# Performance work log

Hardware: AMD Instinct MI355X
Metric: run time of the kernel (lower is better)

The kernel has to match this reference:

```python
import jax, jax.numpy as jnp
import numpy as np
from jax import lax

SEQ, BATCH, INPUT, HIDDEN = 2048, 32, 256, 256


def setup_inputs() -> dict:
    key = jax.random.key(0)
    k1, k2, k3 = jax.random.split(key, 3)
    scale = 1.0 / np.sqrt(HIDDEN)
    return {
        "input": jax.random.normal(k1, (SEQ, BATCH, INPUT), dtype=jnp.float32),
        "W_ih": jax.random.normal(k2, (3 * HIDDEN, INPUT), dtype=jnp.float32) * scale,
        "W_hh": jax.random.normal(k3, (3 * HIDDEN, HIDDEN), dtype=jnp.float32) * scale,
        "b_ih": jnp.zeros((3 * HIDDEN,), dtype=jnp.float32),
        "b_hh": jnp.zeros((3 * HIDDEN,), dtype=jnp.float32),
    }


def reference(input, W_ih, W_hh, b_ih, b_hh):
    """Single-layer unidirectional CustomGRU forward.

    Faithful to the torch module, including its quirk: the n-gate gets the
    W_hh_n @ h contribution twice (once un-gated via `gates`, once gated by r).
    Returns (output [S,B,H], h_n [1,B,H]).
    """
    H = W_hh.shape[0] // 3
    W_hn = W_hh[2 * H:]  # [H, H]
    # Precompute input projections for all timesteps (same math, batched GEMM).
    x_proj = jnp.einsum('sbi,gi->sbg', input, W_ih) + b_ih + b_hh  # [S,B,3H]

    def step(h, xp):
        gates = xp + h @ W_hh.T  # [B, 3H]
        r, z, n = jnp.split(gates, 3, axis=1)
        r = jax.nn.sigmoid(r)
        z = jax.nn.sigmoid(z)
        n = jnp.tanh(n + r * (h @ W_hn.T))
        h_new = (1.0 - z) * n + z * h
        return h_new, h_new

    h0 = jnp.zeros((input.shape[1], H), dtype=input.dtype)
    h_last, output = lax.scan(step, h0, x_proj)
    return output, h_last[None, :, :]
```

## Files before the change

kernel.cpp:

```cpp
#include <hip/hip_runtime.h>
#include <stdint.h>
#include <stddef.h>

#define S_LEN 2048
#define BATCH 32
#define NIN   256
#define NH    256
#define NG    768

typedef _Float16 half2_t __attribute__((ext_vector_type(2)));
typedef _Float16 half8_t __attribute__((ext_vector_type(8)));
typedef int      int16v  __attribute__((ext_vector_type(16)));

#if __has_builtin(__builtin_amdgcn_exp2f)
#define EXP2F(x) __builtin_amdgcn_exp2f(x)
#else
#define EXP2F(x) exp2f(x)
#endif

static __device__ __forceinline__ float fdot2(half2_t a, half2_t b, float c) {
  return __builtin_amdgcn_fdot2(a, b, c, false);
}
static __device__ __forceinline__ half2_t pack2(float lo, float hi) {
  half2_t r; r[0] = (_Float16)lo; r[1] = (_Float16)hi; return r;
}
static __device__ __forceinline__ float sigmoid_fast(float x) {
  float e = EXP2F(-1.44269504088896340736f * x);
  return 1.0f / (1.0f + e);
}
static __device__ __forceinline__ float tanh_fast(float x) {
  float e = EXP2F(2.88539008177792681472f * x);
  return 1.0f - 2.0f / (1.0f + e);
}

static __device__ __forceinline__ float quad_sum(float v) {
  int y1 = __builtin_amdgcn_mov_dpp(__builtin_bit_cast(int, v), 0xB1, 0xF, 0xF, true);
  float s = v + __builtin_bit_cast(float, y1);
  int y2 = __builtin_amdgcn_mov_dpp(__builtin_bit_cast(int, s), 0x4E, 0xF, 0xF, true);
  return s + __builtin_bit_cast(float, y2);
}

#define BH(x)    __builtin_bit_cast(half2_t, (x))
#define BW(W, e) __builtin_bit_cast(half2_t, (int)((W)[e]))

#define DOT16(W, i0) do {                                                     \
    int4 q0 = hls[(i0) + 0], q1 = hls[(i0) + 1];                              \
    int4 q2 = hls[(i0) + 2], q3 = hls[(i0) + 3];                              \
    a0 = fdot2(BW(W, 0),  BH(q0.x), a0); a1 = fdot2(BW(W, 1),  BH(q0.y), a1);\
    a2 = fdot2(BW(W, 2),  BH(q0.z), a2); a3 = fdot2(BW(W, 3),  BH(q0.w), a3);\
    a0 = fdot2(BW(W, 4),  BH(q1.x), a0); a1 = fdot2(BW(W, 5),  BH(q1.y), a1);\
    a2 = fdot2(BW(W, 6),  BH(q1.z), a2); a3 = fdot2(BW(W, 7),  BH(q1.w), a3);\
    a0 = fdot2(BW(W, 8),  BH(q2.x), a0); a1 = fdot2(BW(W, 9),  BH(q2.y), a1);\
    a2 = fdot2(BW(W, 10), BH(q2.z), a2); a3 = fdot2(BW(W, 11), BH(q2.w), a3);\
    a0 = fdot2(BW(W, 12), BH(q3.x), a0); a1 = fdot2(BW(W, 13), BH(q3.y), a1);\
    a2 = fdot2(BW(W, 14), BH(q3.z), a2); a3 = fdot2(BW(W, 15), BH(q3.w), a3);\
  } while (0)

#define DOT6(q, U0, U1, U2, U3, U4, U5, o) do {                               \
    a0 = fdot2(BW(U0,(o)+0), BH(q.x), a0); a1 = fdot2(BW(U1,(o)+0), BH(q.x), a1);\
    a2 = fdot2(BW(U2,(o)+0), BH(q.x), a2); a3 = fdot2(BW(U3,(o)+0), BH(q.x), a3);\
    a4 = fdot2(BW(U4,(o)+0), BH(q.x), a4); a5 = fdot2(BW(U5,(o)+0), BH(q.x), a5);\
    a0 = fdot2(BW(U0,(o)+1), BH(q.y), a0); a1 = fdot2(BW(U1,(o)+1), BH(q.y), a1);\
    a2 = fdot2(BW(U2,(o)+1), BH(q.y), a2); a3 = fdot2(BW(U3,(o)+1), BH(q.y), a3);\
    a4 = fdot2(BW(U4,(o)+1), BH(q.y), a4); a5 = fdot2(BW(U5,(o)+1), BH(q.y), a5);\
    a0 = fdot2(BW(U0,(o)+2), BH(q.z), a0); a1 = fdot2(BW(U1,(o)+2), BH(q.z), a1);\
    a2 = fdot2(BW(U2,(o)+2), BH(q.z), a2); a3 = fdot2(BW(U3,(o)+2), BH(q.z), a3);\
    a4 = fdot2(BW(U4,(o)+2), BH(q.z), a4); a5 = fdot2(BW(U5,(o)+2), BH(q.z), a5);\
    a0 = fdot2(BW(U0,(o)+3), BH(q.w), a0); a1 = fdot2(BW(U1,(o)+3), BH(q.w), a1);\
    a2 = fdot2(BW(U2,(o)+3), BH(q.w), a2); a3 = fdot2(BW(U3,(o)+3), BH(q.w), a3);\
    a4 = fdot2(BW(U4,(o)+3), BH(q.w), a4); a5 = fdot2(BW(U5,(o)+3), BH(q.w), a5);\
  } while (0)

#define LDW(W, o) do {                                                        \
    int4 q0 = wsrc[(o) + 0], q1 = wsrc[(o) + 1];                              \
    int4 q2 = wsrc[(o) + 2], q3 = wsrc[(o) + 3];                              \
    W = (int16v){q0.x, q0.y, q0.z, q0.w, q1.x, q1.y, q1.z, q1.w,              \
                 q2.x, q2.y, q2.z, q2.w, q3.x, q3.y, q3.z, q3.w};             \
  } while (0)

__global__ __launch_bounds__(256) void prep_in_kernel(const float* __restrict__ in,
                                                      _Float16* __restrict__ in16) {
  size_t v = (size_t)blockIdx.x * 256 + threadIdx.x;
  const float4* p4 = (const float4*)in;
  float4 a = p4[v * 2 + 0];
  float4 b = p4[v * 2 + 1];
  half8_t o;
  o[0] = (_Float16)a.x; o[1] = (_Float16)a.y; o[2] = (_Float16)a.z; o[3] = (_Float16)a.w;
  o[4] = (_Float16)b.x; o[5] = (_Float16)b.y; o[6] = (_Float16)b.z; o[7] = (_Float16)b.w;
  ((half8_t*)in16)[v] = o;
}

__global__ __launch_bounds__(256) void prep_w_kernel(const float* __restrict__ W_ih,
                                                     const float* __restrict__ W_hh,
                                                     const float* __restrict__ b_ih,
                                                     const float* __restrict__ b_hh,
                                                     half2_t* __restrict__ whh3,
                                                     half2_t* __restrict__ wih2,
                                                     float* __restrict__ bias) {
  int idx = blockIdx.x * 256 + threadIdx.x;
  if (idx < 128 * NG) {
    int tid = idx / 192;
    int r   = idx - tid * 192;
    int d   = r >> 5, kk = r & 31;
    int gate = d >> 1, jj = d & 1;
    int c  = tid & 3, j1 = tid >> 2;
    int row = gate * NH + 2 * j1 + jj;
    int col = 64 * c + 2 * kk;
    whh3[idx] = pack2(W_hh[(size_t)row * NH + col], W_hh[(size_t)row * NH + col + 1]);
  } else if (idx < 2 * 128 * NG) {
    int i2 = idx - 128 * NG;
    int g = i2 >> 7, kk = i2 & 127;
    wih2[(size_t)g * 128 + kk] = pack2(W_ih[(size_t)g * NIN + 2 * kk], W_ih[(size_t)g * NIN + 2 * kk + 1]);
  } else if (idx < 2 * 128 * NG + NG) {
    int g = idx - 2 * 128 * NG;
    bias[g] = b_ih[g] + b_hh[g];
  }
}

__global__
__attribute__((amdgpu_flat_work_group_size(768, 768), amdgpu_waves_per_eu(3, 3)))
void xproj_kernel(const _Float16* __restrict__ in16,
                  const half2_t* __restrict__ wih2,
                  const float* __restrict__ bias,
                  float* __restrict__ xp_out) {
  __shared__ char occ_pad[86016];
  {
    unsigned lp = (unsigned)(uintptr_t)&occ_pad[0];
    asm volatile("" :: "v"(lp));
  }
  const int g = threadIdx.x;
  const int row0 = blockIdx.x * 64;
  const float bg = bias[g];

  int16v w0, w1, w2, w3, w4, w5, w6, w7;
  {
    const int4* wsrc = (const int4*)(wih2 + (size_t)g * 128);
    LDW(w0, 0);  LDW(w1, 4);  LDW(w2, 8);  LDW(w3, 12);
    LDW(w4, 16); LDW(w5, 20); LDW(w6, 24); LDW(w7, 28);
  }
  asm volatile("" : "+v"(w0), "+v"(w1), "+v"(w2), "+v"(w3),
                    "+v"(w4), "+v"(w5), "+v"(w6), "+v"(w7));

  for (int r = 0; r < 64; ++r) {
    const int row = row0 + r;
    const int4* hls = (const int4*)(in16 + (size_t)row * NIN);
    float a0 = 0.f, a1 = 0.f, a2 = 0.f, a3 = 0.f;
    DOT16(w0, 0);  DOT16(w1, 4);  DOT16(w2, 8);  DOT16(w3, 12);
    DOT16(w4, 16); DOT16(w5, 20); DOT16(w6, 24); DOT16(w7, 28);
    xp_out[(size_t)row * NG + g] = (a0 + a1) + (a2 + a3) + bg;
  }
}

__global__
__attribute__((amdgpu_flat_work_group_size(512, 512), amdgpu_waves_per_eu(2, 2)))
void gru_kernel(const float* __restrict__ xp,
                const half2_t* __restrict__ whh3,
                float* __restrict__ out) {
  const int b   = blockIdx.x;
  const int tid = threadIdx.x;
  const int c   = tid & 3;
  const int j1  = tid >> 2;
  const int jj  = c & 1;
  const int jmine = 2 * j1 + jj;

  int16v W0a, W0b, W1a, W1b, W2a, W2b, W3a, W3b, W4a, W4b, W5a, W5b;
  {
    const int4* wsrc = (const int4*)(whh3 + (size_t)tid * 192);
    LDW(W0a, 0);  LDW(W0b, 4);  LDW(W1a, 8);  LDW(W1b, 12);
    LDW(W2a, 16); LDW(W2b, 20); LDW(W3a, 24); LDW(W3b, 28);
    LDW(W4a, 32); LDW(W4b, 36); LDW(W5a, 40); LDW(W5b, 44);
  }
  asm volatile("" : "+v"(W0a), "+v"(W0b), "+v"(W1a), "+v"(W1b),
                    "+v"(W2a), "+v"(W2b), "+v"(W3a), "+v"(W3b),
                    "+v"(W4a), "+v"(W4b), "+v"(W5a), "+v"(W5b));

  __shared__ __attribute__((aligned(16))) char smh[1152];
  if (tid < 288) ((int*)smh)[tid] = 0;

  const float* xq = xp + (size_t)b * NG + jmine;
  float xr_c = xq[0], xz_c = xq[NH], xn_c = xq[2 * NH];
  xq += (size_t)BATCH * NG;
  float* op = out + (size_t)b * NH + jmine;

  const int wofs = 144 * (jmine >> 6) + 2 * (jmine & 63);

  float h = 0.f;
  __syncthreads();

  for (int t = 0; t < S_LEN; ++t) {
    float xr_n = xq[0], xz_n = xq[NH], xn_n = xq[2 * NH];

    const char* hb = smh + (t & 1) * 576 + c * 144;
    float a0 = 0.f, a1 = 0.f, a2 = 0.f, a3 = 0.f, a4 = 0.f, a5 = 0.f;
    int4 q0 = *(const int4*)(hb +   0), q1 = *(const int4*)(hb +  16);
    int4 q2 = *(const int4*)(hb +  32), q3 = *(const int4*)(hb +  48);
    int4 q4 = *(const int4*)(hb +  64), q5 = *(const int4*)(hb +  80);
    int4 q6 = *(const int4*)(hb +  96), q7 = *(const int4*)(hb + 112);
    DOT6(q0, W0a, W1a, W2a, W3a, W4a, W5a, 0);
    DOT6(q1, W0a, W1a, W2a, W3a, W4a, W5a, 4);
    DOT6(q2, W0a, W1a, W2a, W3a, W4a, W5a, 8);
    DOT6(q3, W0a, W1a, W2a, W3a, W4a, W5a, 12);
    DOT6(q4, W0b, W1b, W2b, W3b, W4b, W5b, 0);
    DOT6(q5, W0b, W1b, W2b, W3b, W4b, W5b, 4);
    DOT6(q6, W0b, W1b, W2b, W3b, W4b, W5b, 8);
    DOT6(q7, W0b, W1b, W2b, W3b, W4b, W5b, 12);

    float s0 = quad_sum(a0), s1 = quad_sum(a1);
    float s2 = quad_sum(a2), s3 = quad_sum(a3);
    float s4 = quad_sum(a4), s5 = quad_sum(a5);
    float mvr = jj ? s1 : s0;
    float mvz = jj ? s3 : s2;
    float mvn = jj ? s5 : s4;

    float r = sigmoid_fast(xr_c + mvr);
    float z = sigmoid_fast(xz_c + mvz);
    float n = tanh_fast(xn_c + mvn + r * mvn);
    h = z * (h - n) + n;

    if (c < 2) {
      op[0] = h;
      *(_Float16*)(smh + (((t + 1) & 1) * 576) + wofs) = (_Float16)h;
    }
    asm volatile("s_waitcnt lgkmcnt(0)\n\ts_barrier" ::: "memory");

    xr_c = xr_n; xz_c = xz_n; xn_c = xn_n;
    xq += (size_t)BATCH * NG;
    op += (size_t)BATCH * NH;
  }

  if (c < 2) out[(size_t)S_LEN * BATCH * NH + (size_t)b * NH + jmine] = h;
}

extern "C" void kernel_launch(void* const* d_in, const int* in_sizes, int n_in,
                              void* d_out, int out_size, void* d_ws, size_t ws_size,
                              hipStream_t stream) {
  const float* input = (const float*)d_in[0];
  const float* W_ih  = (const float*)d_in[1];
  const float* W_hh  = (const float*)d_in[2];
  const float* b_ih  = (const float*)d_in[3];
  const float* b_hh  = (const float*)d_in[4];
  float* out = (float*)d_out;

  const size_t SB = (size_t)S_LEN * BATCH;
  const size_t xp_b   = SB * NG * 4;
  const size_t in16_b = SB * NIN * 2;
  const size_t w_b    = (size_t)128 * NG * 4;

  char* p = (char*)d_ws;
  float*    xp    = (float*)p;                p += xp_b;
  _Float16* in16  = (_Float16*)p;             p += in16_b;
  half2_t*  whh3  = (half2_t*)p;              p += w_b;
  half2_t*  wih2  = (half2_t*)p;              p += w_b;
  float*    bias  = (float*)p;

  prep_in_kernel<<<8192, 256, 0, stream>>>(input, in16);
  prep_w_kernel<<<(2 * 128 * NG + NG + 255) / 256, 256, 0, stream>>>(W_ih, W_hh, b_ih, b_hh,
                                                                     whh3, wih2, bias);
  xproj_kernel<<<1024, 768, 0, stream>>>(in16, wih2, bias, xp);
  gru_kernel<<<BATCH, 512, 0, stream>>>(xp, whh3, out);
  (void)out_size; (void)n_in; (void)in_sizes; (void)ws_size;
}
```

Before: 2.627 ms.

## Fuse input projection into recurrent kernel with flag-based producer/consumer overlap

Merges the input-projection GEMM and the sequential GRU recurrence into one launch. The first 32 blocks run the recurrence, and the remaining 2048 blocks each compute 32 rows of x_proj and then publish a per-timestep-chunk ready flag with a release store. Recurrent blocks poll these flags with system-coherent loads every 8 steps, so the projection work overlaps the serial scan instead of running before it. The projection is rewritten to reuse the recurrent kernel's 4-lane dot-product layout, and the quad reduction is reordered to select before the second DPP step. This relies on the 32 recurrent blocks being scheduled first and staying co-resident to avoid deadlock, and the polling adds memory traffic.

```diff
diff --git a/kernel.cpp b/kernel.cpp
--- a/kernel.cpp
+++ b/kernel.cpp
@@ -7,10 +7,13 @@
 #define NIN   256
 #define NH    256
 #define NG    768
+#define GRUB  32
+#define XPB   2048
 
 typedef _Float16 half2_t __attribute__((ext_vector_type(2)));
 typedef _Float16 half8_t __attribute__((ext_vector_type(8)));
 typedef int      int16v  __attribute__((ext_vector_type(16)));
+typedef int      int4v   __attribute__((ext_vector_type(4)));
 
 #if __has_builtin(__builtin_amdgcn_exp2f)
 #define EXP2F(x) __builtin_amdgcn_exp2f(x)
@@ -32,29 +35,35 @@
   float e = EXP2F(2.88539008177792681472f * x);
   return 1.0f - 2.0f / (1.0f + e);
 }
-
-static __device__ __forceinline__ float quad_sum(float v) {
-  int y1 = __builtin_amdgcn_mov_dpp(__builtin_bit_cast(int, v), 0xB1, 0xF, 0xF, true);
-  float s = v + __builtin_bit_cast(float, y1);
-  int y2 = __builtin_amdgcn_mov_dpp(__builtin_bit_cast(int, s), 0x4E, 0xF, 0xF, true);
-  return s + __builtin_bit_cast(float, y2);
-}
+static __device__ __forceinline__ float dpp_xor1(float v) {
+  return __builtin_bit_cast(float,
+    __builtin_amdgcn_mov_dpp(__builtin_bit_cast(int, v), 0xB1, 0xF, 0xF, true));
+}
+static __device__ __forceinline__ float dpp_xor2(float v) {
+  return __builtin_bit_cast(float,
+    __builtin_amdgcn_mov_dpp(__builtin_bit_cast(int, v), 0x4E, 0xF, 0xF, true));
+}
+
+static __device__ __forceinline__ int flags_all12(const int* p) {
+  int4v a, b, c;
+  asm volatile("global_load_dwordx4 %0, %3, off sc0 sc1\n"
+               "global_load_dwordx4 %1, %4, off sc0 sc1\n"
+               "global_load_dwordx4 %2, %5, off sc0 sc1\n"
+               "s_waitcnt vmcnt(0)"
+               : "=v"(a), "=v"(b), "=v"(c)
+               : "v"(p), "v"(p + 4), "v"(p + 8)
+               : "memory");
+  int all = a.x & a.y & a.z & a.w;
+  all &= b.x & b.y & b.z & b.w;
+  all &= c.x & c.y & c.z & c.w;
+  return all;
+}
+#define FLAGWAIT(BASEP) do {                                                  \
+    while (!flags_all12(BASEP)) __builtin_amdgcn_s_sleep(16);                 \
+  } while (0)
 
 #define BH(x)    __builtin_bit_cast(half2_t, (x))
 #define BW(W, e) __builtin_bit_cast(half2_t, (int)((W)[e]))
-
-#define DOT16(W, i0) do {                                                     \
-    int4 q0 = hls[(i0) + 0], q1 = hls[(i0) + 1];                              \
-    int4 q2 = hls[(i0) + 2], q3 = hls[(i0) + 3];                              \
-    a0 = fdot2(BW(W, 0),  BH(q0.x), a0); a1 = fdot2(BW(W, 1),  BH(q0.y), a1);\
-    a2 = fdot2(BW(W, 2),  BH(q0.z), a2); a3 = fdot2(BW(W, 3),  BH(q0.w), a3);\
-    a0 = fdot2(BW(W, 4),  BH(q1.x), a0); a1 = fdot2(BW(W, 5),  BH(q1.y), a1);\
-    a2 = fdot2(BW(W, 6),  BH(q1.z), a2); a3 = fdot2(BW(W, 7),  BH(q1.w), a3);\
-    a0 = fdot2(BW(W, 8),  BH(q2.x), a0); a1 = fdot2(BW(W, 9),  BH(q2.y), a1);\
-    a2 = fdot2(BW(W, 10), BH(q2.z), a2); a3 = fdot2(BW(W, 11), BH(q2.w), a3);\
-    a0 = fdot2(BW(W, 12), BH(q3.x), a0); a1 = fdot2(BW(W, 13), BH(q3.y), a1);\
-    a2 = fdot2(BW(W, 14), BH(q3.z), a2); a3 = fdot2(BW(W, 15), BH(q3.w), a3);\
-  } while (0)
 
 #define DOT6(q, U0, U1, U2, U3, U4, U5, o) do {                               \
     a0 = fdot2(BW(U0,(o)+0), BH(q.x), a0); a1 = fdot2(BW(U1,(o)+0), BH(q.x), a1);\
@@ -78,9 +87,48 @@
                  q2.x, q2.y, q2.z, q2.w, q3.x, q3.y, q3.z, q3.w};             \
   } while (0)
 
+#define LOADPIN_W(SRC) \
+  int16v W0a, W0b, W1a, W1b, W2a, W2b, W3a, W3b, W4a, W4b, W5a, W5b;         \
+  {                                                                           \
+    const int4* wsrc = (const int4*)(SRC);                                    \
+    LDW(W0a, 0);  LDW(W0b, 4);  LDW(W1a, 8);  LDW(W1b, 12);                   \
+    LDW(W2a, 16); LDW(W2b, 20); LDW(W3a, 24); LDW(W3b, 28);                   \
+    LDW(W4a, 32); LDW(W4b, 36); LDW(W5a, 40); LDW(W5b, 44);                   \
+  }                                                                           \
+  asm volatile("" : "+v"(W0a), "+v"(W0b), "+v"(W1a), "+v"(W1b),               \
+                    "+v"(W2a), "+v"(W2b), "+v"(W3a), "+v"(W3b),               \
+                    "+v"(W4a), "+v"(W4b), "+v"(W5a), "+v"(W5b));
+
+#define DOT6x8() do {                                                         \
+    DOT6(q0, W0a, W1a, W2a, W3a, W4a, W5a, 0);                                \
+    DOT6(q1, W0a, W1a, W2a, W3a, W4a, W5a, 4);                                \
+    DOT6(q2, W0a, W1a, W2a, W3a, W4a, W5a, 8);                                \
+    DOT6(q3, W0a, W1a, W2a, W3a, W4a, W5a, 12);                               \
+    DOT6(q4, W0b, W1b, W2b, W3b, W4b, W5b, 0);                                \
+    DOT6(q5, W0b, W1b, W2b, W3b, W4b, W5b, 4);                                \
+    DOT6(q6, W0b, W1b, W2b, W3b, W4b, W5b, 8);                                \
+    DOT6(q7, W0b, W1b, W2b, W3b, W4b, W5b, 12);                               \
+  } while (0)
+
+#define QREDUCE(MVR, MVZ, MVN) do {                                           \
+    float b0 = a0 + dpp_xor1(a0), b1 = a1 + dpp_xor1(a1);                     \
+    float b2 = a2 + dpp_xor1(a2), b3 = a3 + dpp_xor1(a3);                     \
+    float b4 = a4 + dpp_xor1(a4), b5 = a5 + dpp_xor1(a5);                     \
+    float xr_ = jj ? b1 : b0, xz_ = jj ? b3 : b2, xn_ = jj ? b5 : b4;         \
+    MVR = xr_ + dpp_xor2(xr_);                                                \
+    MVZ = xz_ + dpp_xor2(xz_);                                                \
+    MVN = xn_ + dpp_xor2(xn_);                                                \
+  } while (0)
+
 __global__ __launch_bounds__(256) void prep_in_kernel(const float* __restrict__ in,
-                                                      _Float16* __restrict__ in16) {
+                                                      _Float16* __restrict__ in16,
+                                                      int* __restrict__ flags) {
   size_t v = (size_t)blockIdx.x * 256 + threadIdx.x;
+  if (blockIdx.x < 9) {
+    int i = blockIdx.x * 256 + threadIdx.x;
+    if (i < XPB) flags[i] = 0;
+    else if (i < XPB + 8) flags[i] = 1;
+  }
   const float4* p4 = (const float4*)in;
   float4 a = p4[v * 2 + 0];
   float4 b = p4[v * 2 + 1];
@@ -95,7 +143,7 @@
                                                      const float* __restrict__ b_ih,
                                                      const float* __restrict__ b_hh,
                                                      half2_t* __restrict__ whh3,
-                                                     half2_t* __restrict__ wih2,
+                                                     half2_t* __restrict__ wih3,
                                                      float* __restrict__ bias) {
   int idx = blockIdx.x * 256 + threadIdx.x;
   if (idx < 128 * NG) {
@@ -108,9 +156,15 @@
     int col = 64 * c + 2 * kk;
     whh3[idx] = pack2(W_hh[(size_t)row * NH + col], W_hh[(size_t)row * NH + col + 1]);
   } else if (idx < 2 * 128 * NG) {
-    int i2 = idx - 128 * NG;
-    int g = i2 >> 7, kk = i2 & 127;
-    wih2[(size_t)g * 128 + kk] = pack2(W_ih[(size_t)g * NIN + 2 * kk], W_ih[(size_t)g * NIN + 2 * kk + 1]);
+    int i2  = idx - 128 * NG;
+    int tid = i2 / 192;
+    int r   = i2 - tid * 192;
+    int d   = r >> 5, kk = r & 31;
+    int gate = d >> 1, jj = d & 1;
+    int c  = tid & 3, j1 = tid >> 2;
+    int row = gate * NH + 2 * j1 + jj;
+    int col = 64 * c + 2 * kk;
+    wih3[i2] = pack2(W_ih[(size_t)row * NIN + col], W_ih[(size_t)row * NIN + col + 1]);
   } else if (idx < 2 * 128 * NG + NG) {
     int g = idx - 2 * 128 * NG;
     bias[g] = b_ih[g] + b_hh[g];
@@ -118,64 +172,56 @@
 }
 
 __global__
-__attribute__((amdgpu_flat_work_group_size(768, 768), amdgpu_waves_per_eu(3, 3)))
-void xproj_kernel(const _Float16* __restrict__ in16,
-                  const half2_t* __restrict__ wih2,
+__attribute__((amdgpu_flat_work_group_size(512, 512), amdgpu_waves_per_eu(2, 2)))
+void fused_kernel(const _Float16* __restrict__ in16,
+                  const half2_t* __restrict__ wih3,
                   const float* __restrict__ bias,
-                  float* __restrict__ xp_out) {
-  __shared__ char occ_pad[86016];
-  {
-    unsigned lp = (unsigned)(uintptr_t)&occ_pad[0];
-    asm volatile("" :: "v"(lp));
-  }
-  const int g = threadIdx.x;
-  const int row0 = blockIdx.x * 64;
-  const float bg = bias[g];
-
-  int16v w0, w1, w2, w3, w4, w5, w6, w7;
-  {
-    const int4* wsrc = (const int4*)(wih2 + (size_t)g * 128);
-    LDW(w0, 0);  LDW(w1, 4);  LDW(w2, 8);  LDW(w3, 12);
-    LDW(w4, 16); LDW(w5, 20); LDW(w6, 24); LDW(w7, 28);
-  }
-  asm volatile("" : "+v"(w0), "+v"(w1), "+v"(w2), "+v"(w3),
-                    "+v"(w4), "+v"(w5), "+v"(w6), "+v"(w7));
-
-  for (int r = 0; r < 64; ++r) {
-    const int row = row0 + r;
-    const int4* hls = (const int4*)(in16 + (size_t)row * NIN);
-    float a0 = 0.f, a1 = 0.f, a2 = 0.f, a3 = 0.f;
-    DOT16(w0, 0);  DOT16(w1, 4);  DOT16(w2, 8);  DOT16(w3, 12);
-    DOT16(w4, 16); DOT16(w5, 20); DOT16(w6, 24); DOT16(w7, 28);
-    xp_out[(size_t)row * NG + g] = (a0 + a1) + (a2 + a3) + bg;
-  }
-}
-
-__global__
-__attribute__((amdgpu_flat_work_group_size(512, 512), amdgpu_waves_per_eu(2, 2)))
-void gru_kernel(const float* __restrict__ xp,
-                const half2_t* __restrict__ whh3,
-                float* __restrict__ out) {
-  const int b   = blockIdx.x;
+                  float* __restrict__ xp,
+                  const half2_t* __restrict__ whh3,
+                  float* __restrict__ out,
+                  int* __restrict__ flags) {
   const int tid = threadIdx.x;
   const int c   = tid & 3;
   const int j1  = tid >> 2;
   const int jj  = c & 1;
   const int jmine = 2 * j1 + jj;
 
-  int16v W0a, W0b, W1a, W1b, W2a, W2b, W3a, W3b, W4a, W4b, W5a, W5b;
-  {
-    const int4* wsrc = (const int4*)(whh3 + (size_t)tid * 192);
-    LDW(W0a, 0);  LDW(W0b, 4);  LDW(W1a, 8);  LDW(W1b, 12);
-    LDW(W2a, 16); LDW(W2b, 20); LDW(W3a, 24); LDW(W3b, 28);
-    LDW(W4a, 32); LDW(W4b, 36); LDW(W5a, 40); LDW(W5b, 44);
+  if (blockIdx.x >= GRUB) {
+    const int xb = (int)blockIdx.x - GRUB;
+    LOADPIN_W(wih3 + (size_t)tid * 192);
+    const float bgr = bias[jmine], bgz = bias[NH + jmine], bgn = bias[2 * NH + jmine];
+    const char* inrow = (const char*)(in16 + (size_t)xb * 32 * NIN) + c * 128;
+    float* xo = xp + (size_t)xb * 32 * NG + jmine;
+    for (int rr = 0; rr < 32; ++rr) {
+      float a0 = 0.f, a1 = 0.f, a2 = 0.f, a3 = 0.f, a4 = 0.f, a5 = 0.f;
+      int4 q0 = *(const int4*)(inrow +   0), q1 = *(const int4*)(inrow +  16);
+      int4 q2 = *(const int4*)(inrow +  32), q3 = *(const int4*)(inrow +  48);
+      int4 q4 = *(const int4*)(inrow +  64), q5 = *(const int4*)(inrow +  80);
+      int4 q6 = *(const int4*)(inrow +  96), q7 = *(const int4*)(inrow + 112);
+      DOT6x8();
+      float mvr, mvz, mvn;
+      QREDUCE(mvr, mvz, mvn);
+      if (c < 2) {
+        xo[0]      = mvr + bgr;
+        xo[NH]     = mvz + bgz;
+        xo[2 * NH] = mvn + bgn;
+      }
+      inrow += NIN * 2;
+      xo += NG;
+    }
+    __syncthreads();
+    if (tid == 0)
+      __hip_atomic_store(&flags[xb], 1, __ATOMIC_RELEASE, __HIP_MEMORY_SCOPE_AGENT);
+    return;
   }
-  asm volatile("" : "+v"(W0a), "+v"(W0b), "+v"(W1a), "+v"(W1b),
-                    "+v"(W2a), "+v"(W2b), "+v"(W3a), "+v"(W3b),
-                    "+v"(W4a), "+v"(W4b), "+v"(W5a), "+v"(W5b));
+
+  const int b = blockIdx.x;
+  LOADPIN_W(whh3 + (size_t)tid * 192);
 
   __shared__ __attribute__((aligned(16))) char smh[1152];
   if (tid < 288) ((int*)smh)[tid] = 0;
+
+  FLAGWAIT(flags);
 
   const float* xq = xp + (size_t)b * NG + jmine;
   float xr_c = xq[0], xz_c = xq[NH], xn_c = xq[2 * NH];
@@ -187,46 +233,39 @@
   float h = 0.f;
   __syncthreads();
 
-  for (int t = 0; t < S_LEN; ++t) {
-    float xr_n = xq[0], xz_n = xq[NH], xn_n = xq[2 * NH];
-
-    const char* hb = smh + (t & 1) * 576 + c * 144;
-    float a0 = 0.f, a1 = 0.f, a2 = 0.f, a3 = 0.f, a4 = 0.f, a5 = 0.f;
-    int4 q0 = *(const int4*)(hb +   0), q1 = *(const int4*)(hb +  16);
-    int4 q2 = *(const int4*)(hb +  32), q3 = *(const int4*)(hb +  48);
-    int4 q4 = *(const int4*)(hb +  64), q5 = *(const int4*)(hb +  80);
-    int4 q6 = *(const int4*)(hb +  96), q7 = *(const int4*)(hb + 112);
-    DOT6(q0, W0a, W1a, W2a, W3a, W4a, W5a, 0);
-    DOT6(q1, W0a, W1a, W2a, W3a, W4a, W5a, 4);
-    DOT6(q2, W0a, W1a, W2a, W3a, W4a, W5a, 8);
-    DOT6(q3, W0a, W1a, W2a, W3a, W4a, W5a, 12);
-    DOT6(q4, W0b, W1b, W2b, W3b, W4b, W5b, 0);
-    DOT6(q5, W0b, W1b, W2b, W3b, W4b, W5b, 4);
-    DOT6(q6, W0b, W1b, W2b, W3b, W4b, W5b, 8);
-    DOT6(q7, W0b, W1b, W2b, W3b, W4b, W5b, 12);
-
-    float s0 = quad_sum(a0), s1 = quad_sum(a1);
-    float s2 = quad_sum(a2), s3 = quad_sum(a3);
-    float s4 = quad_sum(a4), s5 = quad_sum(a5);
-    float mvr = jj ? s1 : s0;
-    float mvz = jj ? s3 : s2;
-    float mvn = jj ? s5 : s4;
-
-    float r = sigmoid_fast(xr_c + mvr);
-    float z = sigmoid_fast(xz_c + mvz);
-    float n = tanh_fast(xn_c + mvn + r * mvn);
-    h = z * (h - n) + n;
-
-    if (c < 2) {
-      op[0] = h;
-      *(_Float16*)(smh + (((t + 1) & 1) * 576) + wofs) = (_Float16)h;
+#define GSTEP(RB, WB) do {                                                    \
+    float xr_n = xq[0], xz_n = xq[NH], xn_n = xq[2 * NH];                     \
+    const char* hb = smh + (RB) + c * 144;                                    \
+    float a0 = 0.f, a1 = 0.f, a2 = 0.f, a3 = 0.f, a4 = 0.f, a5 = 0.f;        \
+    int4 q0 = *(const int4*)(hb +   0), q1 = *(const int4*)(hb +  16);       \
+    int4 q2 = *(const int4*)(hb +  32), q3 = *(const int4*)(hb +  48);       \
+    int4 q4 = *(const int4*)(hb +  64), q5 = *(const int4*)(hb +  80);       \
+    int4 q6 = *(const int4*)(hb +  96), q7 = *(const int4*)(hb + 112);       \
+    DOT6x8();                                                                 \
+    float mvr, mvz, mvn;                                                      \
+    QREDUCE(mvr, mvz, mvn);                                                   \
+    float r = sigmoid_fast(xr_c + mvr);                                       \
+    float z = sigmoid_fast(xz_c + mvz);                                       \
+    float n = tanh_fast(xn_c + mvn + r * mvn);              \
+    h = z * (h - n) + n;                                                      \
+    if (c < 2) {                                                              \
+      op[0] = h;                                                              \
+      *(_Float16*)(smh + (WB) + wofs) = (_Float16)h;                          \
+    }                                                                         \
+    asm volatile("s_waitcnt lgkmcnt(0)\n\ts_barrier" ::: "memory");           \
+    xr_c = xr_n; xz_c = xz_n; xn_c = xn_n;                                    \
+    xq += (size_t)BATCH * NG;                                                 \
+    op += (size_t)BATCH * NH;                                                 \
+  } while (0)
+
+  for (int t0 = 0; t0 < S_LEN; t0 += 8) {
+    if (t0) FLAGWAIT(flags + t0);
+    for (int u = 0; u < 4; ++u) {
+      GSTEP(0, 576);
+      GSTEP(576, 0);
     }
-    asm volatile("s_waitcnt lgkmcnt(0)\n\ts_barrier" ::: "memory");
-
-    xr_c = xr_n; xz_c = xz_n; xn_c = xn_n;
-    xq += (size_t)BATCH * NG;
-    op += (size_t)BATCH * NH;
   }
+#undef GSTEP
 
   if (c < 2) out[(size_t)S_LEN * BATCH * NH + (size_t)b * NH + jmine] = h;
 }
@@ -250,13 +289,14 @@
   float*    xp    = (float*)p;                p += xp_b;
   _Float16* in16  = (_Float16*)p;             p += in16_b;
   half2_t*  whh3  = (half2_t*)p;              p += w_b;
-  half2_t*  wih2  = (half2_t*)p;              p += w_b;
-  float*    bias  = (float*)p;
-
-  prep_in_kernel<<<8192, 256, 0, stream>>>(input, in16);
+  half2_t*  wih3  = (half2_t*)p;              p += w_b;
+  float*    bias  = (float*)p;                p += (size_t)NG * 4;
+  uintptr_t fp_ = (((uintptr_t)p) + 127) & ~(uintptr_t)127;
+  int*      flags = (int*)fp_;
+
+  prep_in_kernel<<<8192, 256, 0, stream>>>(input, in16, flags);
   prep_w_kernel<<<(2 * 128 * NG + NG + 255) / 256, 256, 0, stream>>>(W_ih, W_hh, b_ih, b_hh,
-                                                                     whh3, wih2, bias);
-  xproj_kernel<<<1024, 768, 0, stream>>>(in16, wih2, bias, xp);
-  gru_kernel<<<BATCH, 512, 0, stream>>>(xp, whh3, out);
+                                                                     whh3, wih3, bias);
+  fused_kernel<<<GRUB + XPB, 512, 0, stream>>>(in16, wih3, bias, xp, whh3, out, flags);
   (void)out_size; (void)n_in; (void)in_sizes; (void)ws_size;
 }
```

Result: faster. 2.362 ms (-10.1%).
